# Kernel optimization log

Hardware: AMD Instinct MI355X
Metric: run time of the kernel (lower is better)

## Reference

```python
import jax, jax.numpy as jnp
import numpy as np

N, S, I, L, M = 4096, 8, 256, 512, 256


def setup_inputs() -> dict:
    key = jax.random.key(0)
    ks = jax.random.split(key, 13)
    sc_in = 1.0 / np.sqrt(I + L)
    sc_out = 1.0 / np.sqrt(L)
    return {
        "modulation": jax.random.normal(ks[0], (N, S * I), jnp.float32),
        "h0": jax.random.normal(ks[1], (N, S * L), jnp.float32),
        "c0": jax.random.normal(ks[2], (N, S * L), jnp.float32),
        "Wi": jax.random.normal(ks[3], (S, L, I + L), jnp.float32) * sc_in,
        "bi": jnp.full((S, L), -1.0, jnp.float32),  # init_input bias
        "Wf": jax.random.normal(ks[4], (S, L, I + L), jnp.float32) * sc_in,
        "bf": jnp.full((S, L), 1.0, jnp.float32),   # init_forget bias
        "Wg": jax.random.normal(ks[5], (S, L, I + L), jnp.float32) * sc_in,
        "bg": jnp.zeros((S, L), jnp.float32),
        "Wo": jax.random.normal(ks[6], (S, L, I + L), jnp.float32) * sc_in,
        "bo": jnp.zeros((S, L), jnp.float32),
        "Wy": jax.random.normal(ks[7], (S, M, L), jnp.float32) * sc_out,
        "by": jnp.zeros((S, M), jnp.float32),
    }


def reference(modulation, h0, c0, Wi, bi, Wf, bf, Wg, bg, Wo, bo, Wy, by):
    n = modulation.shape[0]
    x = modulation.reshape(n, S, I)          # [N,S,I]
    h = h0.reshape(n, S, L)                  # [N,S,L]
    c = c0.reshape(n, S, L)
    xh = jnp.concatenate([x, h], axis=-1)    # cat_groups: per-stream [x_s, h_s] -> [N,S,I+L]
    # grouped per-stream linear projections for the four gates
    i = jax.nn.sigmoid(jnp.einsum('nsd,sld->nsl', xh, Wi) + bi)
    f = jax.nn.sigmoid(jnp.einsum('nsd,sld->nsl', xh, Wf) + bf)
    g = jnp.tanh(jnp.einsum('nsd,sld->nsl', xh, Wg) + bg)
    o = jax.nn.sigmoid(jnp.einsum('nsd,sld->nsl', xh, Wo) + bo)
    c_new = f * c + i * g
    h_new = o * jnp.tanh(c_new)              # dropout p=0 -> identity
    y = jnp.einsum('nsl,sml->nsm', h_new, Wy) + by
    return y.reshape(n, S * M)
```

## Files before the change

kernel.cpp:

```cpp
#include <hip/hip_runtime.h>
#include <stdint.h>

#define S_ 8
#define N_ 4096
#define I_ 256
#define L_ 512
#define M_ 256
#define D_ 768
#define NT32 24

typedef __bf16 bf16x8 __attribute__((ext_vector_type(8)));
typedef float f32x4 __attribute__((ext_vector_type(4)));
typedef unsigned short ushort_t;

__device__ __forceinline__ unsigned short f2bf(float f) {
  union { float f; uint32_t u; } c; c.f = f;
  uint32_t u = c.u;
  uint32_t r = u + 0x7FFFu + ((u >> 16) & 1u);
  return (unsigned short)(r >> 16);
}

__device__ __forceinline__ float fsigmoid(float x) {
  return 1.0f / (1.0f + __expf(-x));
}
__device__ __forceinline__ float ftanh(float x) {
  float ax = fabsf(x);
  float e = __expf(-2.0f * ax);
  float t = (1.0f - e) / (1.0f + e);
  return copysignf(t, x);
}

#define GLD16(gsrc, ldst)                                                                  \
  __builtin_amdgcn_global_load_lds(                                                        \
      (const __attribute__((address_space(1))) uint32_t*)(uintptr_t)(gsrc),                \
      (__attribute__((address_space(3))) uint32_t*)(uintptr_t)(ldst), 16, 0, 0)


__global__ __launch_bounds__(256) void cast5_kernel(
    const float* __restrict__ Wi, const float* __restrict__ Wf,
    const float* __restrict__ Wg, const float* __restrict__ Wo,
    const float* __restrict__ Wy, ushort_t* __restrict__ w4,
    ushort_t* __restrict__ wyb) {
  const int y = blockIdx.y;
  const int GW = S_ * L_ * D_ / 4;
  const float* src;
  ushort_t* dst;
  int n4;
  if (y < 4) {
    src = (y == 0) ? Wi : (y == 1) ? Wf : (y == 2) ? Wg : Wo;
    dst = w4 + (size_t)y * S_ * L_ * D_;
    n4 = GW;
  } else {
    src = Wy; dst = wyb; n4 = S_ * M_ * L_ / 4;
  }
  int t = blockIdx.x * 256 + threadIdx.x;
  int stride = gridDim.x * 256;
  for (; t < n4; t += stride) {
    float4 v = ((const float4*)src)[t];
    ushort4 o;
    o.x = f2bf(v.x); o.y = f2bf(v.y); o.z = f2bf(v.z); o.w = f2bf(v.w);
    ((ushort4*)dst)[t] = o;
  }
}

__global__ __launch_bounds__(256) void build_xh_kernel(const float* __restrict__ mod,
                                                       const float* __restrict__ h0,
                                                       ushort_t* __restrict__ xh) {
  const int y = blockIdx.y;
  int t = blockIdx.x * 256 + threadIdx.x;
  int stride = gridDim.x * 256;
  if (y == 0) {
    const int total = S_ * N_ * (I_ / 4);
    for (; t < total; t += stride) {
      int r = t >> 6, c = t & 63;
      int s = r >> 12, n = r & (N_ - 1);
      float4 v = *(const float4*)(mod + (size_t)n * (S_ * I_) + s * I_ + c * 4);
      ushort4 o;
      o.x = f2bf(v.x); o.y = f2bf(v.y); o.z = f2bf(v.z); o.w = f2bf(v.w);
      *(ushort4*)(xh + (size_t)r * D_ + c * 4) = o;
    }
  } else {
    const int total = S_ * N_ * (L_ / 4);
    for (; t < total; t += stride) {
      int r = t >> 7, c = t & 127;
      int s = r >> 12, n = r & (N_ - 1);
      float4 v = *(const float4*)(h0 + (size_t)n * (S_ * L_) + s * L_ + c * 4);
      ushort4 o;
      o.x = f2bf(v.x); o.y = f2bf(v.y); o.z = f2bf(v.z); o.w = f2bf(v.w);
      *(ushort4*)(xh + (size_t)r * D_ + I_ + c * 4) = o;
    }
  }
}


__global__ __launch_bounds__(1024, 4) void gates_kernel(
    const ushort_t* __restrict__ xh,
    const ushort_t* __restrict__ w4,
    const float* __restrict__ bi, const float* __restrict__ bff,
    const float* __restrict__ bg, const float* __restrict__ bo,
    const float* __restrict__ c0,
    ushort_t* __restrict__ hout)
{
  __shared__ __align__(16) ushort_t smem[32768];
  const int tid = threadIdx.x;
  const int lane = tid & 63;
  const int ln15 = lane & 15;
  const int ln4 = lane >> 4;
  const int w = tid >> 6;
  const int wm = w >> 2;
  const int wl = w & 3;

  const int bid = blockIdx.x;
  const int s = bid & 7;
  const int r = bid >> 3;
  const int n0 = (r >> 3) << 8;
  const int l0 = (r & 7) << 6;

  const size_t xh_base = (size_t)(s * N_ + n0) * D_;

  const int sr_s = tid >> 3;
  const int ch0_s = (tid & 7) ^ (sr_s & 7);
  const int rr_s = (sr_s << 1) | (ch0_s >> 2);
  const int c_s = ch0_s & 3;
  const ushort_t* aSrcBase = xh + xh_base + (size_t)rr_s * D_ + (c_s << 3);
  const int gB = rr_s >> 6, llB = rr_s & 63;
  const ushort_t* bSrcBase = w4 + ((size_t)((gB * S_ + s) * L_) + l0 + llB) * D_ + (c_s << 3);
  const int ldsSlot = (w << 6) * 8;

  f32x4 acc[4][4];
  #pragma unroll
  for (int i = 0; i < 4; ++i)
    #pragma unroll
    for (int j = 0; j < 4; ++j) {
      f32x4 z = {0.f, 0.f, 0.f, 0.f};
      acc[i][j] = z;
    }

#define STAGE(bufA, tile) do {                                                          \
    int k0_ = (tile) << 5;                                                              \
    GLD16(aSrcBase + k0_, &smem[((bufA) + (w << 6)) * 8]);                              \
    GLD16(bSrcBase + k0_, &smem[((bufA) + 1024 + (w << 6)) * 8]);                       \
  } while (0)

  STAGE(0, 0);
  asm volatile("s_waitcnt vmcnt(0)" ::: "memory");
  __syncthreads();

  for (int t = 0; t < NT32; ++t) {
    const int cur = (t & 1) << 11;
    const int nxt = cur ^ 2048;
    if (t < NT32 - 1) STAGE(nxt, t + 1);

    bf16x8 a[4];
    #pragma unroll
    for (int rt = 0; rt < 4; ++rt) {
      int rr = (wm << 6) + (rt << 4) + ln15;
      int sr = rr >> 1;
      int ch = (((rr & 1) << 2) | ln4) ^ (sr & 7);
      a[rt] = *(const bf16x8*)&smem[(cur + (sr << 3) + ch) * 8];
    }
    bf16x8 b[4];
    #pragma unroll
    for (int cj = 0; cj < 4; ++cj) {
      int rB = (cj << 6) + (wl << 4) + ln15;
      int sr = rB >> 1;
      int ch = (((rB & 1) << 2) | ln4) ^ (sr & 7);
      b[cj] = *(const bf16x8*)&smem[(cur + 1024 + (sr << 3) + ch) * 8];
    }
    #pragma unroll
    for (int rt = 0; rt < 4; ++rt)
      #pragma unroll
      for (int cj = 0; cj < 4; ++cj)
        acc[rt][cj] = __builtin_amdgcn_mfma_f32_16x16x32_bf16(a[rt], b[cj], acc[rt][cj], 0, 0, 0);

    asm volatile("s_waitcnt vmcnt(0)" ::: "memory");
    __syncthreads();
  }

  const int l = l0 + (wl << 4) + ln15;
  const float vbi = bi[s * L_ + l];
  const float vbf = bff[s * L_ + l];
  const float vbg = bg[s * L_ + l];
  const float vbo = bo[s * L_ + l];
  #pragma unroll
  for (int rt = 0; rt < 4; ++rt) {
    #pragma unroll
    for (int j = 0; j < 4; ++j) {
      const int n = n0 + (wm << 6) + (rt << 4) + (ln4 << 2) + j;
      const float c0v = c0[(size_t)n * (S_ * L_) + s * L_ + l];
      const float iv = fsigmoid(acc[rt][0][j] + vbi);
      const float fv = fsigmoid(acc[rt][1][j] + vbf);
      const float gv = ftanh(acc[rt][2][j] + vbg);
      const float ov = fsigmoid(acc[rt][3][j] + vbo);
      const float cn = fv * c0v + iv * gv;
      const float hn = ov * ftanh(cn);
      hout[(size_t)(s * N_ + n) * L_ + l] = f2bf(hn);
    }
  }
#undef STAGE
}

__global__ __launch_bounds__(256, 2) void out_kernel(
    const ushort_t* __restrict__ h,
    const ushort_t* __restrict__ wy,
    const float* __restrict__ by,
    float* __restrict__ out)
{
  __shared__ __align__(16) ushort_t smem[1536 * 8];
  const int tid = threadIdx.x;
  const int lane = tid & 63;
  const int w = tid >> 6;
  const int n0 = blockIdx.x * 128;
  const int m0 = blockIdx.y * 64;
  const int s = blockIdx.z;

  f32x4 acc[2][4];
  #pragma unroll
  for (int rt = 0; rt < 2; ++rt)
    #pragma unroll
    for (int ct = 0; ct < 4; ++ct) {
      f32x4 z = {0.f, 0.f, 0.f, 0.f};
      acc[rt][ct] = z;
    }

  const size_t h_row0 = (size_t)(s * N_ + n0) * L_;

  for (int t = 0; t < L_ / 64; ++t) {
    const int k0 = t * 64;
    #pragma unroll
    for (int it = 0; it < 4; ++it) {
      int chunk = it * 256 + tid;
      int r = chunk >> 3, c = chunk & 7;
      int cg = c ^ (r & 7);
      const ushort_t* src = h + h_row0 + (size_t)r * L_ + k0 + cg * 8;
      GLD16(src, &smem[(it * 256 + w * 64) * 8]);
    }
    #pragma unroll
    for (int it = 0; it < 2; ++it) {
      int chunk = it * 256 + tid;
      int rl = chunk >> 3, c = chunk & 7;
      int cg = c ^ (rl & 7);
      const ushort_t* src = wy + ((size_t)(s * M_ + m0 + rl)) * L_ + k0 + cg * 8;
      GLD16(src, &smem[(1024 + it * 256 + w * 64) * 8]);
    }
    __syncthreads();
    #pragma unroll
    for (int kk = 0; kk < 2; ++kk) {
      const int cc = kk * 4 + (lane >> 4);
      bf16x8 av[2];
      #pragma unroll
      for (int rt = 0; rt < 2; ++rt) {
        int rr = w * 32 + rt * 16 + (lane & 15);
        av[rt] = *(const bf16x8*)&smem[(rr * 8 + (cc ^ (rr & 7))) * 8];
      }
      #pragma unroll
      for (int ct = 0; ct < 4; ++ct) {
        int rl = ct * 16 + (lane & 15);
        bf16x8 b = *(const bf16x8*)&smem[(1024 + rl * 8 + (cc ^ (rl & 7))) * 8];
        acc[0][ct] = __builtin_amdgcn_mfma_f32_16x16x32_bf16(av[0], b, acc[0][ct], 0, 0, 0);
        acc[1][ct] = __builtin_amdgcn_mfma_f32_16x16x32_bf16(av[1], b, acc[1][ct], 0, 0, 0);
      }
    }
    __syncthreads();
  }

  #pragma unroll
  for (int ct = 0; ct < 4; ++ct) {
    const int m = m0 + ct * 16 + (lane & 15);
    const float vb = by[s * M_ + m];
    #pragma unroll
    for (int rt = 0; rt < 2; ++rt) {
      #pragma unroll
      for (int j = 0; j < 4; ++j) {
        const int n = n0 + w * 32 + rt * 16 + (lane >> 4) * 4 + j;
        out[(size_t)n * (S_ * M_) + s * M_ + m] = acc[rt][ct][j] + vb;
      }
    }
  }
}


extern "C" void kernel_launch(void* const* d_in, const int* in_sizes, int n_in,
                              void* d_out, int out_size, void* d_ws, size_t ws_size,
                              hipStream_t stream) {
  const float* mod = (const float*)d_in[0];
  const float* h0  = (const float*)d_in[1];
  const float* c0  = (const float*)d_in[2];
  const float* Wi  = (const float*)d_in[3];
  const float* bi  = (const float*)d_in[4];
  const float* Wf  = (const float*)d_in[5];
  const float* bf  = (const float*)d_in[6];
  const float* Wg  = (const float*)d_in[7];
  const float* bg  = (const float*)d_in[8];
  const float* Wo  = (const float*)d_in[9];
  const float* bo  = (const float*)d_in[10];
  const float* Wy  = (const float*)d_in[11];
  const float* by  = (const float*)d_in[12];
  float* out = (float*)d_out;

  ushort_t* ws = (ushort_t*)d_ws;
  ushort_t* xh   = ws;
  ushort_t* w4   = xh  + (size_t)S_ * N_ * D_;
  ushort_t* wyb  = w4  + (size_t)4 * S_ * L_ * D_;
  ushort_t* hbuf = wyb + (size_t)S_ * M_ * L_;

  cast5_kernel<<<dim3(512, 5), 256, 0, stream>>>(Wi, Wf, Wg, Wo, Wy, w4, wyb);
  build_xh_kernel<<<dim3(2048, 2), 256, 0, stream>>>(mod, h0, xh);
  gates_kernel<<<1024, 1024, 0, stream>>>(xh, w4, bi, bf, bg, bo, c0, hbuf);
  out_kernel<<<dim3(N_ / 128, M_ / 64, S_), 256, 0, stream>>>(hbuf, wyb, by, out);
}
```

Before: 207.1 us.

## Restructure gates GEMM into 512-thread blocks with 64-wide K and multi-stage pipelining

The gates kernel moves from 1024-thread blocks with 32-wide K tiles and a full vmcnt(0) wait each step to 512-thread blocks where each wave computes 8x4 MFMA tiles, twice as many per wave. K is split into 64-wide steps made of two halves, and loads are staged into separate A/B regions of a doubled LDS buffer. Global prefetches are issued between MFMA quarters, with partial vmcnt waits, sched barriers and setprio. The aim is to overlap global-to-LDS copies with MFMA work and to improve register-level reuse. The cost is more accumulator registers, more LDS, and more barriers per step.

```diff
diff --git a/kernel.cpp b/kernel.cpp
--- a/kernel.cpp
+++ b/kernel.cpp
@@ -7,7 +7,7 @@
 #define L_ 512
 #define M_ 256
 #define D_ 768
-#define NT32 24
+#define NT64 12
 
 typedef __bf16 bf16x8 __attribute__((ext_vector_type(8)));
 typedef float f32x4 __attribute__((ext_vector_type(4)));
@@ -92,8 +92,7 @@
   }
 }
 
-
-__global__ __launch_bounds__(1024, 4) void gates_kernel(
+__global__ __launch_bounds__(512, 2) void gates_kernel(
     const ushort_t* __restrict__ xh,
     const ushort_t* __restrict__ w4,
     const float* __restrict__ bi, const float* __restrict__ bff,
@@ -101,14 +100,14 @@
     const float* __restrict__ c0,
     ushort_t* __restrict__ hout)
 {
-  __shared__ __align__(16) ushort_t smem[32768];
+  __shared__ __align__(16) ushort_t smem[65536];
   const int tid = threadIdx.x;
   const int lane = tid & 63;
   const int ln15 = lane & 15;
   const int ln4 = lane >> 4;
   const int w = tid >> 6;
   const int wm = w >> 2;
-  const int wl = w & 3;
+  const int wn = w & 3;
 
   const int bid = blockIdx.x;
   const int s = bid & 7;
@@ -122,71 +121,130 @@
   const int ch0_s = (tid & 7) ^ (sr_s & 7);
   const int rr_s = (sr_s << 1) | (ch0_s >> 2);
   const int c_s = ch0_s & 3;
-  const ushort_t* aSrcBase = xh + xh_base + (size_t)rr_s * D_ + (c_s << 3);
+  const ushort_t* aSrc0 = xh + xh_base + (size_t)rr_s * D_ + (c_s << 3);
+  const ushort_t* aSrc1 = aSrc0 + (size_t)128 * D_;
   const int gB = rr_s >> 6, llB = rr_s & 63;
-  const ushort_t* bSrcBase = w4 + ((size_t)((gB * S_ + s) * L_) + l0 + llB) * D_ + (c_s << 3);
-  const int ldsSlot = (w << 6) * 8;
-
-  f32x4 acc[4][4];
+  const ushort_t* bSrc0 = w4 + ((size_t)((gB * S_ + s) * L_) + l0 + llB) * D_ + (c_s << 3);
+  const ushort_t* bSrc1 = bSrc0 + (size_t)2 * S_ * L_ * D_;
+
+#define REGB(P, kh, isB) (((P) << 12) + ((kh) << 11) + ((isB) << 10))
+
+#define STAGE_R(P, kh, isB, tile) do {                                                  \
+    const int off_ = ((tile) << 6) + ((kh) << 5);                                       \
+    if (isB) {                                                                          \
+      GLD16(bSrc0 + off_, &smem[(REGB(P, kh, 1) + (w << 6)) * 8]);                      \
+      GLD16(bSrc1 + off_, &smem[(REGB(P, kh, 1) + 512 + (w << 6)) * 8]);                \
+    } else {                                                                            \
+      GLD16(aSrc0 + off_, &smem[(REGB(P, kh, 0) + (w << 6)) * 8]);                      \
+      GLD16(aSrc1 + off_, &smem[(REGB(P, kh, 0) + 512 + (w << 6)) * 8]);                \
+    }                                                                                   \
+  } while (0)
+
+#define LOAD_A(P, kh, rtb) do {                                                         \
+    _Pragma("unroll")                                                                   \
+    for (int q_ = 0; q_ < 4; ++q_) {                                                    \
+      int rr_ = (wm << 7) + (((rtb) + q_) << 4) + ln15;                                 \
+      int sr_ = rr_ >> 1;                                                               \
+      int ch_ = (((rr_ & 1) << 2) | ln4) ^ (sr_ & 7);                                   \
+      a[q_] = *(const bf16x8*)&smem[(REGB(P, kh, 0) + (sr_ << 3) + ch_) * 8];           \
+    }                                                                                   \
+  } while (0)
+
+#define LOAD_B(P, kh) do {                                                              \
+    _Pragma("unroll")                                                                   \
+    for (int g_ = 0; g_ < 4; ++g_) {                                                    \
+      int rB_ = (g_ << 6) + (wn << 4) + ln15;                                           \
+      int sr_ = rB_ >> 1;                                                               \
+      int ch_ = (((rB_ & 1) << 2) | ln4) ^ (sr_ & 7);                                   \
+      bb[g_] = *(const bf16x8*)&smem[(REGB(P, kh, 1) + (sr_ << 3) + ch_) * 8];          \
+    }                                                                                   \
+  } while (0)
+
+#define MFMA_Q(rtb) do {                                                                \
+    _Pragma("unroll")                                                                   \
+    for (int q_ = 0; q_ < 4; ++q_)                                                      \
+      _Pragma("unroll")                                                                 \
+      for (int g_ = 0; g_ < 4; ++g_)                                                    \
+        acc[(rtb) + q_][g_] = __builtin_amdgcn_mfma_f32_16x16x32_bf16(                  \
+            a[q_], bb[g_], acc[(rtb) + q_][g_], 0, 0, 0);                               \
+  } while (0)
+
+#define BAR() __builtin_amdgcn_s_barrier()
+#define SB0() __builtin_amdgcn_sched_barrier(0)
+#define LGKM0() do { asm volatile("s_waitcnt lgkmcnt(0)"); SB0(); } while (0)
+#define VMC8() do { asm volatile("s_waitcnt vmcnt(8)" ::: "memory"); SB0(); } while (0)
+
+  f32x4 acc[8][4];
   #pragma unroll
-  for (int i = 0; i < 4; ++i)
+  for (int i = 0; i < 8; ++i)
     #pragma unroll
     for (int j = 0; j < 4; ++j) {
       f32x4 z = {0.f, 0.f, 0.f, 0.f};
       acc[i][j] = z;
     }
 
-#define STAGE(bufA, tile) do {                                                          \
-    int k0_ = (tile) << 5;                                                              \
-    GLD16(aSrcBase + k0_, &smem[((bufA) + (w << 6)) * 8]);                              \
-    GLD16(bSrcBase + k0_, &smem[((bufA) + 1024 + (w << 6)) * 8]);                       \
-  } while (0)
-
-  STAGE(0, 0);
+  STAGE_R(0, 0, 0, 0);
+  STAGE_R(0, 0, 1, 0);
+  STAGE_R(0, 1, 0, 0);
+  STAGE_R(0, 1, 1, 0);
+  STAGE_R(1, 0, 0, 1);
+  STAGE_R(1, 0, 1, 1);
+  VMC8();
+  BAR();
+
+  for (int T = 0; T < NT64; ++T) {
+    const int P = T & 1;
+    const int Q = P ^ 1;
+    const int Tp1 = (T + 1 < NT64) ? T + 1 : NT64 - 1;
+    const int Tp2 = (T + 2 < NT64) ? T + 2 : NT64 - 1;
+    bf16x8 a[4];
+    bf16x8 bb[4];
+
+    LOAD_A(P, 0, 0);
+    LOAD_B(P, 0);
+    STAGE_R(Q, 1, 0, Tp1);
+    BAR();
+    LGKM0();
+    __builtin_amdgcn_s_setprio(1); MFMA_Q(0); __builtin_amdgcn_s_setprio(0);
+    SB0();
+    BAR();
+    LOAD_A(P, 0, 4);
+    STAGE_R(Q, 1, 1, Tp1);
+    BAR();
+    LGKM0();
+    __builtin_amdgcn_s_setprio(1); MFMA_Q(4); __builtin_amdgcn_s_setprio(0);
+    SB0();
+    VMC8();
+    BAR();
+    LOAD_A(P, 1, 0);
+    LOAD_B(P, 1);
+    STAGE_R(P, 0, 0, Tp2);
+    BAR();
+    LGKM0();
+    __builtin_amdgcn_s_setprio(1); MFMA_Q(0); __builtin_amdgcn_s_setprio(0);
+    SB0();
+    BAR();
+    LOAD_A(P, 1, 4);
+    STAGE_R(P, 0, 1, Tp2);
+    BAR();
+    LGKM0();
+    __builtin_amdgcn_s_setprio(1); MFMA_Q(4); __builtin_amdgcn_s_setprio(0);
+    SB0();
+    VMC8();
+    BAR();
+  }
   asm volatile("s_waitcnt vmcnt(0)" ::: "memory");
-  __syncthreads();
-
-  for (int t = 0; t < NT32; ++t) {
-    const int cur = (t & 1) << 11;
-    const int nxt = cur ^ 2048;
-    if (t < NT32 - 1) STAGE(nxt, t + 1);
-
-    bf16x8 a[4];
-    #pragma unroll
-    for (int rt = 0; rt < 4; ++rt) {
-      int rr = (wm << 6) + (rt << 4) + ln15;
-      int sr = rr >> 1;
-      int ch = (((rr & 1) << 2) | ln4) ^ (sr & 7);
-      a[rt] = *(const bf16x8*)&smem[(cur + (sr << 3) + ch) * 8];
-    }
-    bf16x8 b[4];
-    #pragma unroll
-    for (int cj = 0; cj < 4; ++cj) {
-      int rB = (cj << 6) + (wl << 4) + ln15;
-      int sr = rB >> 1;
-      int ch = (((rB & 1) << 2) | ln4) ^ (sr & 7);
-      b[cj] = *(const bf16x8*)&smem[(cur + 1024 + (sr << 3) + ch) * 8];
-    }
-    #pragma unroll
-    for (int rt = 0; rt < 4; ++rt)
-      #pragma unroll
-      for (int cj = 0; cj < 4; ++cj)
-        acc[rt][cj] = __builtin_amdgcn_mfma_f32_16x16x32_bf16(a[rt], b[cj], acc[rt][cj], 0, 0, 0);
-
-    asm volatile("s_waitcnt vmcnt(0)" ::: "memory");
-    __syncthreads();
-  }
-
-  const int l = l0 + (wl << 4) + ln15;
+
+  const int l = l0 + (wn << 4) + ln15;
   const float vbi = bi[s * L_ + l];
   const float vbf = bff[s * L_ + l];
   const float vbg = bg[s * L_ + l];
   const float vbo = bo[s * L_ + l];
   #pragma unroll
-  for (int rt = 0; rt < 4; ++rt) {
+  for (int rt = 0; rt < 8; ++rt) {
     #pragma unroll
     for (int j = 0; j < 4; ++j) {
-      const int n = n0 + (wm << 6) + (rt << 4) + (ln4 << 2) + j;
+      const int n = n0 + (wm << 7) + (rt << 4) + (ln4 << 2) + j;
       const float c0v = c0[(size_t)n * (S_ * L_) + s * L_ + l];
       const float iv = fsigmoid(acc[rt][0][j] + vbi);
       const float fv = fsigmoid(acc[rt][1][j] + vbf);
@@ -197,7 +255,11 @@
       hout[(size_t)(s * N_ + n) * L_ + l] = f2bf(hn);
     }
   }
-#undef STAGE
+#undef STAGE_R
+#undef LOAD_A
+#undef LOAD_B
+#undef MFMA_Q
+#undef REGB
 }
 
 __global__ __launch_bounds__(256, 2) void out_kernel(
@@ -230,9 +292,9 @@
     #pragma unroll
     for (int it = 0; it < 4; ++it) {
       int chunk = it * 256 + tid;
-      int r = chunk >> 3, c = chunk & 7;
-      int cg = c ^ (r & 7);
-      const ushort_t* src = h + h_row0 + (size_t)r * L_ + k0 + cg * 8;
+      int rr = chunk >> 3, c = chunk & 7;
+      int cg = c ^ (rr & 7);
+      const ushort_t* src = h + h_row0 + (size_t)rr * L_ + k0 + cg * 8;
       GLD16(src, &smem[(it * 256 + w * 64) * 8]);
     }
     #pragma unroll
@@ -306,6 +368,6 @@
 
   cast5_kernel<<<dim3(512, 5), 256, 0, stream>>>(Wi, Wf, Wg, Wo, Wy, w4, wyb);
   build_xh_kernel<<<dim3(2048, 2), 256, 0, stream>>>(mod, h0, xh);
-  gates_kernel<<<1024, 1024, 0, stream>>>(xh, w4, bi, bf, bg, bo, c0, hbuf);
+  gates_kernel<<<1024, 512, 0, stream>>>(xh, w4, bi, bf, bg, bo, c0, hbuf);
   out_kernel<<<dim3(N_ / 128, M_ / 64, S_), 256, 0, stream>>>(hbuf, wyb, by, out);
 }
```

After: 215.5 us. +4.1%, slower.

## Restructure gates GEMM: 512 threads, B in registers, deeper A prefetch

Applied to the files above, without the earlier changes.

The gates kernel drops from 1024 to 512 threads per block, and each wave now computes 128 rows by 4 gates (8x4 MFMA tiles) instead of 64 rows. The weight (B) fragments are loaded straight from global memory into registers, so only the activation tile is staged through LDS, which halves LDS use. Loads are prefetched two tiles ahead with a partial vmcnt wait, split barriers and raised priority during the MFMA phase, so global loads overlap with math. The cost is a much higher register count (32 accumulator tiles plus two register B buffers) and possible spilling or lower occupancy.

```diff
diff --git a/kernel.cpp b/kernel.cpp
--- a/kernel.cpp
+++ b/kernel.cpp
@@ -92,8 +92,7 @@
   }
 }
 
-
-__global__ __launch_bounds__(1024, 4) void gates_kernel(
+__global__ __launch_bounds__(512) void gates_kernel(
     const ushort_t* __restrict__ xh,
     const ushort_t* __restrict__ w4,
     const float* __restrict__ bi, const float* __restrict__ bff,
@@ -101,14 +100,14 @@
     const float* __restrict__ c0,
     ushort_t* __restrict__ hout)
 {
-  __shared__ __align__(16) ushort_t smem[32768];
+  __shared__ __align__(16) ushort_t smem[16384];
   const int tid = threadIdx.x;
   const int lane = tid & 63;
   const int ln15 = lane & 15;
   const int ln4 = lane >> 4;
   const int w = tid >> 6;
   const int wm = w >> 2;
-  const int wl = w & 3;
+  const int wc = w & 3;
 
   const int bid = blockIdx.x;
   const int s = bid & 7;
@@ -122,71 +121,88 @@
   const int ch0_s = (tid & 7) ^ (sr_s & 7);
   const int rr_s = (sr_s << 1) | (ch0_s >> 2);
   const int c_s = ch0_s & 3;
-  const ushort_t* aSrcBase = xh + xh_base + (size_t)rr_s * D_ + (c_s << 3);
-  const int gB = rr_s >> 6, llB = rr_s & 63;
-  const ushort_t* bSrcBase = w4 + ((size_t)((gB * S_ + s) * L_) + l0 + llB) * D_ + (c_s << 3);
-  const int ldsSlot = (w << 6) * 8;
-
-  f32x4 acc[4][4];
-  #pragma unroll
-  for (int i = 0; i < 4; ++i)
+  const ushort_t* aSrc0 = xh + xh_base + (size_t)rr_s * D_ + (c_s << 3);
+  const ushort_t* aSrc1 = aSrc0 + (size_t)128 * D_;
+
+  const ushort_t* bRow[4];
+  #pragma unroll
+  for (int g = 0; g < 4; ++g)
+    bRow[g] = w4 + ((size_t)((g * S_ + s) * L_) + l0 + (wc << 4) + ln15) * D_ + (ln4 << 3);
+
+  f32x4 acc[8][4];
+  #pragma unroll
+  for (int i = 0; i < 8; ++i)
     #pragma unroll
     for (int j = 0; j < 4; ++j) {
       f32x4 z = {0.f, 0.f, 0.f, 0.f};
       acc[i][j] = z;
     }
 
-#define STAGE(bufA, tile) do {                                                          \
-    int k0_ = (tile) << 5;                                                              \
-    GLD16(aSrcBase + k0_, &smem[((bufA) + (w << 6)) * 8]);                              \
-    GLD16(bSrcBase + k0_, &smem[((bufA) + 1024 + (w << 6)) * 8]);                       \
+#define STAGE_A(base, tile) do {                                                        \
+    const int k0_ = (tile) << 5;                                                        \
+    GLD16(aSrc0 + k0_, &smem[((base) + (w << 6)) * 8]);                                 \
+    GLD16(aSrc1 + k0_, &smem[((base) + 512 + (w << 6)) * 8]);                           \
   } while (0)
 
-  STAGE(0, 0);
+#define BLOAD(dst, tile) do {                                                           \
+    const int k0_ = (tile) << 5;                                                        \
+    _Pragma("unroll")                                                                   \
+    for (int g_ = 0; g_ < 4; ++g_) dst[g_] = *(const bf16x8*)(bRow[g_] + k0_);          \
+  } while (0)
+
+#define ITER(T, base, bc) do {                                                          \
+    asm volatile("s_waitcnt vmcnt(10)" ::: "memory");       \
+    __builtin_amdgcn_s_barrier();                           \
+    __builtin_amdgcn_sched_barrier(0);                                                  \
+    bf16x8 a_[8];                                                                       \
+    _Pragma("unroll")                                                                   \
+    for (int rt_ = 0; rt_ < 8; ++rt_) {                                                 \
+      int rr_ = (wm << 7) + (rt_ << 4) + ln15;                                          \
+      int sr_ = rr_ >> 1;                                                               \
+      int ch_ = (((rr_ & 1) << 2) | ln4) ^ (sr_ & 7);                                   \
+      a_[rt_] = *(const bf16x8*)&smem[((base) + (sr_ << 3) + ch_) * 8];                 \
+    }                                                                                   \
+    __builtin_amdgcn_s_setprio(1);                                                      \
+    _Pragma("unroll")                                                                   \
+    for (int rt_ = 0; rt_ < 8; ++rt_)                                                   \
+      _Pragma("unroll")                                                                 \
+      for (int g_ = 0; g_ < 4; ++g_)                                                    \
+        acc[rt_][g_] = __builtin_amdgcn_mfma_f32_16x16x32_bf16(                         \
+            a_[rt_], bc[g_], acc[rt_][g_], 0, 0, 0);                                    \
+    __builtin_amdgcn_s_setprio(0);                                                      \
+    __builtin_amdgcn_sched_barrier(0);                                                  \
+    __builtin_amdgcn_s_barrier();                          \
+    __builtin_amdgcn_sched_barrier(0);                                                  \
+    const int t2_ = ((T) + 2 < NT32) ? (T) + 2 : NT32 - 1;                              \
+    STAGE_A(base, t2_);                                        \
+    BLOAD(bc, t2_);                                         \
+    __builtin_amdgcn_sched_barrier(0);                                                  \
+  } while (0)
+
+  bf16x8 bA[4], bB[4];
+  STAGE_A(0, 0);
+  STAGE_A(1024, 1);
+  BLOAD(bA, 0);
+  BLOAD(bB, 1);
+
+  #pragma unroll 1
+  for (int tt = 0; tt < NT32 / 2; ++tt) {
+    const int T0 = tt << 1;
+    ITER(T0, 0, bA);
+    ITER(T0 + 1, 1024, bB);
+  }
   asm volatile("s_waitcnt vmcnt(0)" ::: "memory");
-  __syncthreads();
-
-  for (int t = 0; t < NT32; ++t) {
-    const int cur = (t & 1) << 11;
-    const int nxt = cur ^ 2048;
-    if (t < NT32 - 1) STAGE(nxt, t + 1);
-
-    bf16x8 a[4];
-    #pragma unroll
-    for (int rt = 0; rt < 4; ++rt) {
-      int rr = (wm << 6) + (rt << 4) + ln15;
-      int sr = rr >> 1;
-      int ch = (((rr & 1) << 2) | ln4) ^ (sr & 7);
-      a[rt] = *(const bf16x8*)&smem[(cur + (sr << 3) + ch) * 8];
-    }
-    bf16x8 b[4];
-    #pragma unroll
-    for (int cj = 0; cj < 4; ++cj) {
-      int rB = (cj << 6) + (wl << 4) + ln15;
-      int sr = rB >> 1;
-      int ch = (((rB & 1) << 2) | ln4) ^ (sr & 7);
-      b[cj] = *(const bf16x8*)&smem[(cur + 1024 + (sr << 3) + ch) * 8];
-    }
-    #pragma unroll
-    for (int rt = 0; rt < 4; ++rt)
-      #pragma unroll
-      for (int cj = 0; cj < 4; ++cj)
-        acc[rt][cj] = __builtin_amdgcn_mfma_f32_16x16x32_bf16(a[rt], b[cj], acc[rt][cj], 0, 0, 0);
-
-    asm volatile("s_waitcnt vmcnt(0)" ::: "memory");
-    __syncthreads();
-  }
-
-  const int l = l0 + (wl << 4) + ln15;
+
+  const int l = l0 + (wc << 4) + ln15;
   const float vbi = bi[s * L_ + l];
   const float vbf = bff[s * L_ + l];
   const float vbg = bg[s * L_ + l];
   const float vbo = bo[s * L_ + l];
   #pragma unroll
-  for (int rt = 0; rt < 4; ++rt) {
+  for (int rt = 0; rt < 8; ++rt) {
     #pragma unroll
     for (int j = 0; j < 4; ++j) {
-      const int n = n0 + (wm << 6) + (rt << 4) + (ln4 << 2) + j;
+      const int n = n0 + (wm << 7) + (rt << 4) + (ln4 << 2) + j;
       const float c0v = c0[(size_t)n * (S_ * L_) + s * L_ + l];
       const float iv = fsigmoid(acc[rt][0][j] + vbi);
       const float fv = fsigmoid(acc[rt][1][j] + vbf);
@@ -197,7 +213,9 @@
       hout[(size_t)(s * N_ + n) * L_ + l] = f2bf(hn);
     }
   }
-#undef STAGE
+#undef ITER
+#undef BLOAD
+#undef STAGE_A
 }
 
 __global__ __launch_bounds__(256, 2) void out_kernel(
@@ -230,9 +248,9 @@
     #pragma unroll
     for (int it = 0; it < 4; ++it) {
       int chunk = it * 256 + tid;
-      int r = chunk >> 3, c = chunk & 7;
-      int cg = c ^ (r & 7);
-      const ushort_t* src = h + h_row0 + (size_t)r * L_ + k0 + cg * 8;
+      int rr = chunk >> 3, c = chunk & 7;
+      int cg = c ^ (rr & 7);
+      const ushort_t* src = h + h_row0 + (size_t)rr * L_ + k0 + cg * 8;
       GLD16(src, &smem[(it * 256 + w * 64) * 8]);
     }
     #pragma unroll
@@ -306,6 +324,6 @@
 
   cast5_kernel<<<dim3(512, 5), 256, 0, stream>>>(Wi, Wf, Wg, Wo, Wy, w4, wyb);
   build_xh_kernel<<<dim3(2048, 2), 256, 0, stream>>>(mod, h0, xh);
-  gates_kernel<<<1024, 1024, 0, stream>>>(xh, w4, bi, bf, bg, bo, c0, hbuf);
+  gates_kernel<<<1024, 512, 0, stream>>>(xh, w4, bi, bf, bg, bo, c0, hbuf);
   out_kernel<<<dim3(N_ / 128, M_ / 64, S_), 256, 0, stream>>>(hbuf, wyb, by, out);
 }
```

New measurement: 269.9 us. +30.3%, slower.

## Double K-tile depth in gates GEMM and merge prep kernels into one launch

Applied to the files above, without the earlier changes.

The gates GEMM now stages 64-wide K tiles instead of 32-wide ones. This halves the number of loop iterations and barriers, at the cost of doubling LDS to 128 KB per block, which may limit occupancy. The weight cast and xh build kernels are merged into a single prep launch with a 7-row grid, removing one kernel launch and letting the two workloads overlap.

```diff
diff --git a/kernel.cpp b/kernel.cpp
--- a/kernel.cpp
+++ b/kernel.cpp
@@ -7,7 +7,7 @@
 #define L_ 512
 #define M_ 256
 #define D_ 768
-#define NT32 24
+#define NT64 12
 
 typedef __bf16 bf16x8 __attribute__((ext_vector_type(8)));
 typedef float f32x4 __attribute__((ext_vector_type(4)));
@@ -35,41 +35,34 @@
       (const __attribute__((address_space(1))) uint32_t*)(uintptr_t)(gsrc),                \
       (__attribute__((address_space(3))) uint32_t*)(uintptr_t)(ldst), 16, 0, 0)
 
-
-__global__ __launch_bounds__(256) void cast5_kernel(
+__global__ __launch_bounds__(256) void prep_kernel(
+    const float* __restrict__ mod, const float* __restrict__ h0,
     const float* __restrict__ Wi, const float* __restrict__ Wf,
     const float* __restrict__ Wg, const float* __restrict__ Wo,
     const float* __restrict__ Wy, ushort_t* __restrict__ w4,
-    ushort_t* __restrict__ wyb) {
-  const int y = blockIdx.y;
-  const int GW = S_ * L_ * D_ / 4;
-  const float* src;
-  ushort_t* dst;
-  int n4;
-  if (y < 4) {
-    src = (y == 0) ? Wi : (y == 1) ? Wf : (y == 2) ? Wg : Wo;
-    dst = w4 + (size_t)y * S_ * L_ * D_;
-    n4 = GW;
-  } else {
-    src = Wy; dst = wyb; n4 = S_ * M_ * L_ / 4;
-  }
-  int t = blockIdx.x * 256 + threadIdx.x;
-  int stride = gridDim.x * 256;
-  for (; t < n4; t += stride) {
-    float4 v = ((const float4*)src)[t];
-    ushort4 o;
-    o.x = f2bf(v.x); o.y = f2bf(v.y); o.z = f2bf(v.z); o.w = f2bf(v.w);
-    ((ushort4*)dst)[t] = o;
-  }
-}
-
-__global__ __launch_bounds__(256) void build_xh_kernel(const float* __restrict__ mod,
-                                                       const float* __restrict__ h0,
-                                                       ushort_t* __restrict__ xh) {
+    ushort_t* __restrict__ wyb, ushort_t* __restrict__ xh) {
   const int y = blockIdx.y;
   int t = blockIdx.x * 256 + threadIdx.x;
-  int stride = gridDim.x * 256;
-  if (y == 0) {
+  const int stride = gridDim.x * 256;
+  if (y < 4) {
+    const float* src = (y == 0) ? Wi : (y == 1) ? Wf : (y == 2) ? Wg : Wo;
+    ushort_t* dst = w4 + (size_t)y * S_ * L_ * D_;
+    const int n4 = S_ * L_ * D_ / 4;
+    for (; t < n4; t += stride) {
+      float4 v = ((const float4*)src)[t];
+      ushort4 o;
+      o.x = f2bf(v.x); o.y = f2bf(v.y); o.z = f2bf(v.z); o.w = f2bf(v.w);
+      ((ushort4*)dst)[t] = o;
+    }
+  } else if (y == 4) {
+    const int n4 = S_ * M_ * L_ / 4;
+    for (; t < n4; t += stride) {
+      float4 v = ((const float4*)Wy)[t];
+      ushort4 o;
+      o.x = f2bf(v.x); o.y = f2bf(v.y); o.z = f2bf(v.z); o.w = f2bf(v.w);
+      ((ushort4*)wyb)[t] = o;
+    }
+  } else if (y == 5) {
     const int total = S_ * N_ * (I_ / 4);
     for (; t < total; t += stride) {
       int r = t >> 6, c = t & 63;
@@ -92,7 +85,6 @@
   }
 }
 
-
 __global__ __launch_bounds__(1024, 4) void gates_kernel(
     const ushort_t* __restrict__ xh,
     const ushort_t* __restrict__ w4,
@@ -101,7 +93,7 @@
     const float* __restrict__ c0,
     ushort_t* __restrict__ hout)
 {
-  __shared__ __align__(16) ushort_t smem[32768];
+  __shared__ __align__(16) ushort_t smem[65536];
   const int tid = threadIdx.x;
   const int lane = tid & 63;
   const int ln15 = lane & 15;
@@ -118,14 +110,25 @@
 
   const size_t xh_base = (size_t)(s * N_ + n0) * D_;
 
-  const int sr_s = tid >> 3;
-  const int ch0_s = (tid & 7) ^ (sr_s & 7);
-  const int rr_s = (sr_s << 1) | (ch0_s >> 2);
-  const int c_s = ch0_s & 3;
-  const ushort_t* aSrcBase = xh + xh_base + (size_t)rr_s * D_ + (c_s << 3);
-  const int gB = rr_s >> 6, llB = rr_s & 63;
-  const ushort_t* bSrcBase = w4 + ((size_t)((gB * S_ + s) * L_) + l0 + llB) * D_ + (c_s << 3);
-  const int ldsSlot = (w << 6) * 8;
+  const ushort_t* aSrc[2];
+  const ushort_t* bSrc[2];
+  #pragma unroll
+  for (int rd = 0; rd < 2; ++rd) {
+    int slot = tid + (rd << 10);
+    int row = slot >> 3;
+    int cg = (slot & 7) ^ (row & 7);
+    aSrc[rd] = xh + xh_base + (size_t)row * D_ + (cg << 3);
+    int g = row >> 6, ll = row & 63;
+    bSrc[rd] = w4 + ((size_t)((g * S_ + s) * L_) + l0 + ll) * D_ + (cg << 3);
+  }
+
+#define STAGE(base, tile) do {                                                          \
+    const int k0_ = (tile) << 6;                                                        \
+    GLD16(aSrc[0] + k0_, &smem[((base) + (w << 6)) * 8]);                               \
+    GLD16(aSrc[1] + k0_, &smem[((base) + 1024 + (w << 6)) * 8]);                        \
+    GLD16(bSrc[0] + k0_, &smem[((base) + 2048 + (w << 6)) * 8]);                        \
+    GLD16(bSrc[1] + k0_, &smem[((base) + 3072 + (w << 6)) * 8]);                        \
+  } while (0)
 
   f32x4 acc[4][4];
   #pragma unroll
@@ -136,42 +139,36 @@
       acc[i][j] = z;
     }
 
-#define STAGE(bufA, tile) do {                                                          \
-    int k0_ = (tile) << 5;                                                              \
-    GLD16(aSrcBase + k0_, &smem[((bufA) + (w << 6)) * 8]);                              \
-    GLD16(bSrcBase + k0_, &smem[((bufA) + 1024 + (w << 6)) * 8]);                       \
-  } while (0)
-
   STAGE(0, 0);
   asm volatile("s_waitcnt vmcnt(0)" ::: "memory");
   __syncthreads();
 
-  for (int t = 0; t < NT32; ++t) {
-    const int cur = (t & 1) << 11;
-    const int nxt = cur ^ 2048;
-    if (t < NT32 - 1) STAGE(nxt, t + 1);
-
-    bf16x8 a[4];
-    #pragma unroll
-    for (int rt = 0; rt < 4; ++rt) {
-      int rr = (wm << 6) + (rt << 4) + ln15;
-      int sr = rr >> 1;
-      int ch = (((rr & 1) << 2) | ln4) ^ (sr & 7);
-      a[rt] = *(const bf16x8*)&smem[(cur + (sr << 3) + ch) * 8];
-    }
-    bf16x8 b[4];
-    #pragma unroll
-    for (int cj = 0; cj < 4; ++cj) {
-      int rB = (cj << 6) + (wl << 4) + ln15;
-      int sr = rB >> 1;
-      int ch = (((rB & 1) << 2) | ln4) ^ (sr & 7);
-      b[cj] = *(const bf16x8*)&smem[(cur + 1024 + (sr << 3) + ch) * 8];
-    }
-    #pragma unroll
-    for (int rt = 0; rt < 4; ++rt)
-      #pragma unroll
-      for (int cj = 0; cj < 4; ++cj)
-        acc[rt][cj] = __builtin_amdgcn_mfma_f32_16x16x32_bf16(a[rt], b[cj], acc[rt][cj], 0, 0, 0);
+  #pragma unroll 1
+  for (int t = 0; t < NT64; ++t) {
+    const int cur = (t & 1) << 12;
+    if (t + 1 < NT64) STAGE(cur ^ 4096, t + 1);
+
+    #pragma unroll
+    for (int kk = 0; kk < 2; ++kk) {
+      const int ch = (kk << 2) + ln4;
+      bf16x8 a[4];
+      #pragma unroll
+      for (int rt = 0; rt < 4; ++rt) {
+        int ra = (wm << 6) + (rt << 4) + ln15;
+        a[rt] = *(const bf16x8*)&smem[(cur + (ra << 3) + (ch ^ (ra & 7))) * 8];
+      }
+      bf16x8 b[4];
+      #pragma unroll
+      for (int g = 0; g < 4; ++g) {
+        int rB = (g << 6) + (wl << 4) + ln15;
+        b[g] = *(const bf16x8*)&smem[(cur + 2048 + (rB << 3) + (ch ^ (rB & 7))) * 8];
+      }
+      #pragma unroll
+      for (int rt = 0; rt < 4; ++rt)
+        #pragma unroll
+        for (int g = 0; g < 4; ++g)
+          acc[rt][g] = __builtin_amdgcn_mfma_f32_16x16x32_bf16(a[rt], b[g], acc[rt][g], 0, 0, 0);
+    }
 
     asm volatile("s_waitcnt vmcnt(0)" ::: "memory");
     __syncthreads();
@@ -230,9 +227,9 @@
     #pragma unroll
     for (int it = 0; it < 4; ++it) {
       int chunk = it * 256 + tid;
-      int r = chunk >> 3, c = chunk & 7;
-      int cg = c ^ (r & 7);
-      const ushort_t* src = h + h_row0 + (size_t)r * L_ + k0 + cg * 8;
+      int rr = chunk >> 3, c = chunk & 7;
+      int cg = c ^ (rr & 7);
+      const ushort_t* src = h + h_row0 + (size_t)rr * L_ + k0 + cg * 8;
       GLD16(src, &smem[(it * 256 + w * 64) * 8]);
     }
     #pragma unroll
@@ -304,8 +301,7 @@
   ushort_t* wyb  = w4  + (size_t)4 * S_ * L_ * D_;
   ushort_t* hbuf = wyb + (size_t)S_ * M_ * L_;
 
-  cast5_kernel<<<dim3(512, 5), 256, 0, stream>>>(Wi, Wf, Wg, Wo, Wy, w4, wyb);
-  build_xh_kernel<<<dim3(2048, 2), 256, 0, stream>>>(mod, h0, xh);
+  prep_kernel<<<dim3(768, 7), 256, 0, stream>>>(mod, h0, Wi, Wf, Wg, Wo, Wy, w4, wyb, xh);
   gates_kernel<<<1024, 1024, 0, stream>>>(xh, w4, bi, bf, bg, bo, c0, hbuf);
   out_kernel<<<dim3(N_ / 128, M_ / 64, S_), 256, 0, stream>>>(hbuf, wyb, by, out);
 }
```

New measurement: 197.8 us. -4.5%, faster.
